# Optimization experiments

Hardware: AMD Instinct MI355X
Metric: run time of the kernel (lower is better)

The kernel has to match this reference:

```python
import jax, jax.numpy as jnp
import numpy as np

D_MODEL = 1024
N_HEADS = 16
D_FF = 4096
EPS = 1e-6


def _linear_params(key, d_in, d_out):
    kw, kb = jax.random.split(key)
    bound = 1.0 / np.sqrt(d_in)
    W = jax.random.uniform(kw, (d_out, d_in), minval=-bound, maxval=bound, dtype=jnp.float32)
    b = jax.random.uniform(kb, (d_out,), minval=-bound, maxval=bound, dtype=jnp.float32)
    return W, b


def setup_inputs() -> dict:
    key = jax.random.key(0)
    keys = jax.random.split(key, 8)
    x = jax.random.normal(keys[0], (4, 2048, D_MODEL), dtype=jnp.float32)
    mask = jnp.ones((4, 1, 1, 2048), dtype=jnp.bool_)
    Wq, bq = _linear_params(keys[1], D_MODEL, D_MODEL)
    Wk, bk = _linear_params(keys[2], D_MODEL, D_MODEL)
    Wv, bv = _linear_params(keys[3], D_MODEL, D_MODEL)
    Wo, bo = _linear_params(keys[4], D_MODEL, D_MODEL)
    W1, b1 = _linear_params(keys[5], D_MODEL, D_FF)
    W2, b2 = _linear_params(keys[6], D_FF, D_MODEL)
    ln1_g = jnp.ones((D_MODEL,), jnp.float32); ln1_b = jnp.zeros((D_MODEL,), jnp.float32)
    ln2_g = jnp.ones((D_MODEL,), jnp.float32); ln2_b = jnp.zeros((D_MODEL,), jnp.float32)
    return {"x": x, "mask": mask,
            "Wq": Wq, "bq": bq, "Wk": Wk, "bk": bk, "Wv": Wv, "bv": bv,
            "Wo": Wo, "bo": bo, "W1": W1, "b1": b1, "W2": W2, "b2": b2,
            "ln1_g": ln1_g, "ln1_b": ln1_b, "ln2_g": ln2_g, "ln2_b": ln2_b}


def _layernorm(x, g, b):
    # torch LayerNorm here uses unbiased std and divides by (std + eps)
    mean = jnp.mean(x, axis=-1, keepdims=True)
    std = jnp.std(x, axis=-1, keepdims=True, ddof=1)
    return g * (x - mean) / (std + EPS) + b


def _gelu_tanh(x):
    c = np.sqrt(2.0 / np.pi).astype(np.float32)
    return 0.5 * x * (1.0 + jnp.tanh(c * (x + 0.044715 * x * x * x)))


def _mha(xn, mask, Wq, bq, Wk, bk, Wv, bv, Wo, bo):
    B, S, D = xn.shape
    d_k = D // N_HEADS
    def proj(W, b):
        y = jnp.einsum('bsd,ed->bse', xn, W) + b
        return y.reshape(B, S, N_HEADS, d_k).transpose(0, 2, 1, 3)  # [B,h,S,d_k]
    q, k, v = proj(Wq, bq), proj(Wk, bk), proj(Wv, bv)
    scores = jnp.einsum('bhqd,bhkd->bhqk', q, k) / np.float32(np.sqrt(d_k))
    scores = jnp.where(mask, scores, jnp.float32(-1e9))
    p = jax.nn.softmax(scores, axis=-1)
    o = jnp.einsum('bhqk,bhkd->bhqd', p, v)
    o = o.transpose(0, 2, 1, 3).reshape(B, S, D)
    return jnp.einsum('bsd,ed->bse', o, Wo) + bo


def reference(x, mask, Wq, bq, Wk, bk, Wv, bv, Wo, bo, W1, b1, W2, b2,
              ln1_g, ln1_b, ln2_g, ln2_b):
    xn = _layernorm(x, ln1_g, ln1_b)
    y = x + _mha(xn, mask, Wq, bq, Wk, bk, Wv, bv, Wo, bo)
    yn = _layernorm(y, ln2_g, ln2_b)
    h = _gelu_tanh(jnp.einsum('bsd,fd->bsf', yn, W1) + b1)
    z = y + (jnp.einsum('bsf,df->bsd', h, W2) + b2)
    return z
```

## Files before the change

### kernel.cpp

```cpp
#include <hip/hip_runtime.h>

typedef __bf16 bf16;
typedef __bf16 bfx4 __attribute__((ext_vector_type(4)));
typedef __bf16 bfx8 __attribute__((ext_vector_type(8)));
typedef float  fx4  __attribute__((ext_vector_type(4)));

#define NTOK 8192
#define DM   1024
#define DFF  4096
#define SEQ  2048
#define NH   16
#define DK   64

#define OFF_WQKV 0ull
#define OFF_WO   (OFF_WQKV + 3072ull*1024*2)
#define OFF_W1   (OFF_WO   + 1024ull*1024*2)
#define OFF_W2   (OFF_W1   + 4096ull*1024*2)
#define OFF_BQKV (OFF_W2   + 4096ull*1024*2)
#define OFF_XN   (OFF_BQKV + 3072ull*4)
#define OFF_QKV  (OFF_XN   + 8192ull*1024*2)
#define OFF_ATTN (OFF_QKV  + 8192ull*3072*2)
#define OFF_Y    (OFF_ATTN + 8192ull*1024*2)
#define OFF_VT   OFF_Y
#define OFF_H    OFF_XN
#define OFF_YN   OFF_ATTN

#define BARRIER() do { asm volatile("" ::: "memory"); \
                       __builtin_amdgcn_s_barrier();  \
                       asm volatile("" ::: "memory"); } while (0)

__device__ __forceinline__ void gload16(const void* g, void* l) {
  __builtin_amdgcn_global_load_lds(
      (__attribute__((address_space(1))) void*)(g),
      (__attribute__((address_space(3))) void*)(l), 16, 0, 0);
}

__device__ __forceinline__ float gelu_tanh(float x) {
  float u = 0.7978845608028654f * (x + 0.044715f * x * x * x);
  float t = 1.f - 2.f / (__expf(2.f * u) + 1.f);
  return 0.5f * x * (1.f + t);
}

__global__ __launch_bounds__(256) void cast_all(const float* __restrict__ Wq,
                                                const float* __restrict__ Wk,
                                                const float* __restrict__ Wv,
                                                const float* __restrict__ Wo,
                                                const float* __restrict__ W1,
                                                const float* __restrict__ W2,
                                                bf16* __restrict__ dst) {
  const int bid = blockIdx.x;
  const int g = bid >> 9;
  const int j = ((bid & 511) << 11) + threadIdx.x * 8;
  const float* s;
  if (g == 0) s = Wq;
  else if (g == 1) s = Wk;
  else if (g == 2) s = Wv;
  else if (g == 3) s = Wo;
  else if (g < 8) s = W1 + (size_t)(g - 4) * 1048576;
  else s = W2 + (size_t)(g - 8) * 1048576;
  const float4 a = *(const float4*)(s + j);
  const float4 c = *(const float4*)(s + j + 4);
  bfx8 o;
  o[0] = (bf16)a.x; o[1] = (bf16)a.y; o[2] = (bf16)a.z; o[3] = (bf16)a.w;
  o[4] = (bf16)c.x; o[5] = (bf16)c.y; o[6] = (bf16)c.z; o[7] = (bf16)c.w;
  *(bfx8*)(dst + (size_t)g * 1048576 + j) = o;
}

__global__ void biask(const float* __restrict__ bq, const float* __restrict__ bk,
                      const float* __restrict__ bv, float* __restrict__ o) {
  const int i = blockIdx.x * 1024 + threadIdx.x;
  const float* s = blockIdx.x == 0 ? bq : (blockIdx.x == 1 ? bk : bv);
  o[i] = s[threadIdx.x];
}

__global__ __launch_bounds__(256) void ln_kernel(const float* __restrict__ x,
                                                 const float* __restrict__ g,
                                                 const float* __restrict__ b,
                                                 bf16* __restrict__ out) {
  const int row = blockIdx.x;
  const int c = threadIdx.x * 4;
  const float4 v = *(const float4*)&x[(size_t)row * DM + c];
  float s1 = v.x + v.y + v.z + v.w;
  float s2 = v.x * v.x + v.y * v.y + v.z * v.z + v.w * v.w;
  #pragma unroll
  for (int o = 32; o; o >>= 1) { s1 += __shfl_xor(s1, o); s2 += __shfl_xor(s2, o); }
  __shared__ float red[8];
  const int wid = threadIdx.x >> 6;
  if ((threadIdx.x & 63) == 0) { red[wid] = s1; red[4 + wid] = s2; }
  __syncthreads();
  s1 = red[0] + red[1] + red[2] + red[3];
  s2 = red[4] + red[5] + red[6] + red[7];
  const float mean = s1 * (1.f / (float)DM);
  const float var = (s2 - (float)DM * mean * mean) * (1.f / (float)(DM - 1));
  const float inv = 1.f / (sqrtf(fmaxf(var, 0.f)) + 1e-6f);
  bfx4 o;
  o[0] = (bf16)(g[c + 0] * (v.x - mean) * inv + b[c + 0]);
  o[1] = (bf16)(g[c + 1] * (v.y - mean) * inv + b[c + 1]);
  o[2] = (bf16)(g[c + 2] * (v.z - mean) * inv + b[c + 2]);
  o[3] = (bf16)(g[c + 3] * (v.w - mean) * inv + b[c + 3]);
  *(bfx4*)&out[(size_t)row * DM + c] = o;
}

template <int NREP, int EPI, int VSPLIT>
__global__ __launch_bounds__(512, 2) void gemm256(const bf16* __restrict__ A,
                                                  const bf16* __restrict__ B,
                                                  const float* __restrict__ bias,
                                                  const float* __restrict__ resid,
                                                  bf16* __restrict__ vt,
                                                  void* __restrict__ outp,
                                                  int M, int N, int K) {
  extern __shared__ char lds[];
  constexpr int BHALF = NREP * 4096;
  const int tid = threadIdx.x;
  const int lane = tid & 63, w = tid >> 6;
  const int l15 = lane & 15, lhi = lane >> 4;
  const int wm = w >> 2, wn = w & 3;

  const int nwg = gridDim.x * gridDim.y;
  int bid = blockIdx.y * gridDim.x + blockIdx.x;
  bid = (bid & 7) * (nwg >> 3) + (bid >> 3);
  const int m0 = (bid % gridDim.x) * 256;
  const int n0 = (bid / gridDim.x) * (NREP * 64);

  const char* Ab = (const char*)A;
  const char* Bb = (const char*)B;
  const size_t str = (size_t)K * 2;

  const int r_s = tid >> 3;
  const int c2  = (tid & 7) * 16;
  const int csw = c2 ^ ((r_s & 7) << 4);

  auto stA = [&](int buf, int half, int kt) {
    const size_t kb = (size_t)kt * 128;
    #pragma unroll
    for (int s = 0; s < 2; ++s)
      gload16(Ab + (size_t)(m0 + half * 128 + s * 64 + r_s) * str + kb + csw,
              lds + (buf * 2 + half) * 16384 + s * 8192 + tid * 16);
  };
  auto stB = [&](int buf, int half, int kt) {
    const size_t kb = (size_t)kt * 128;
    #pragma unroll
    for (int s = 0; s < NREP / 2; ++s)
      gload16(Bb + (size_t)(n0 + half * (NREP * 32) + s * 64 + r_s) * str + kb + csw,
              lds + 65536 + (buf * 2 + half) * BHALF + s * 8192 + tid * 16);
  };

  fx4 acc[8][NREP] = {};
  bfx8 af[4][2];
  bfx8 bfv[NREP][2];
  const int asw = (l15 & 7) << 4;

  auto ldA = [&](int buf, int i0) {
    const char* base = lds + (buf * 2 + wm) * 16384;
    #pragma unroll
    for (int ii = 0; ii < 4; ++ii) {
      const int r = (i0 + ii) * 16 + l15;
      #pragma unroll
      for (int kk = 0; kk < 2; ++kk)
        af[ii][kk] = *(const bfx8*)(base + r * 128 + ((kk * 64 + lhi * 16) ^ asw));
    }
  };
  auto ldB = [&](int buf, int j0) {
    const char* base = lds + 65536 + (buf * 2 + (wn >> 1)) * BHALF;
    #pragma unroll
    for (int jj = 0; jj < NREP / 2; ++jj) {
      const int r = (wn & 1) * (NREP * 16) + (j0 + jj) * 16 + l15;
      #pragma unroll
      for (int kk = 0; kk < 2; ++kk)
        bfv[j0 + jj][kk] = *(const bfx8*)(base + r * 128 + ((kk * 64 + lhi * 16) ^ asw));
    }
  };
  auto mm = [&](int qm, int qn) {
    __builtin_amdgcn_s_setprio(1);
    #pragma unroll
    for (int ii = 0; ii < 4; ++ii)
      #pragma unroll
      for (int jj = 0; jj < NREP / 2; ++jj)
        #pragma unroll
        for (int kk = 0; kk < 2; ++kk)
          acc[qm * 4 + ii][qn * (NREP / 2) + jj] =
              __builtin_amdgcn_mfma_f32_16x16x32_bf16(
                  af[ii][kk], bfv[qn * (NREP / 2) + jj][kk],
                  acc[qm * 4 + ii][qn * (NREP / 2) + jj], 0, 0, 0);
    __builtin_amdgcn_s_setprio(0);
  };

  const int nK = K >> 6, niters = nK >> 1;

  stA(0, 0, 0); stA(0, 1, 0); stB(0, 0, 0); stB(0, 1, 0);
  stB(1, 0, 1); stB(1, 1, 1);
  asm volatile("s_waitcnt vmcnt(%0)" :: "i"(NREP) : "memory");
  BARRIER();

  #pragma unroll 1
  for (int it = 0; it < niters; ++it) {
    const int t1 = 2 * it + 1, t2 = 2 * it + 2, t3 = 2 * it + 3;
    const bool more = (it < niters - 1);
    ldA(0, 0); ldB(0, 0);
    stA(1, 0, t1);
    BARRIER(); mm(0, 0); BARRIER();
    ldB(0, NREP / 2);
    stA(1, 1, t1);
    BARRIER(); mm(0, 1); BARRIER();
    ldA(0, 4);
    if (more) stB(0, 0, t2);
    BARRIER(); mm(1, 0); BARRIER();
    if (more) {
      stB(0, 1, t2);
      asm volatile("s_waitcnt vmcnt(%0)" :: "i"(NREP) : "memory");
    } else {
      asm volatile("s_waitcnt vmcnt(0)" ::: "memory");
    }
    BARRIER(); mm(1, 1); BARRIER();
    ldA(1, 0); ldB(1, 0);
    if (more) stA(0, 0, t2);
    BARRIER(); mm(0, 0); BARRIER();
    ldB(1, NREP / 2);
    if (more) stA(0, 1, t2);
    BARRIER(); mm(0, 1); BARRIER();
    ldA(1, 4);
    if (more) stB(1, 0, t3);
    BARRIER(); mm(1, 0); BARRIER();
    if (more) {
      stB(1, 1, t3);
      asm volatile("s_waitcnt vmcnt(%0)" :: "i"(NREP) : "memory");
    }
    BARRIER(); mm(1, 1); BARRIER();
  }

  const int rb = m0 + wm * 128 + lhi * 4;
  const int cb = n0 + wn * 16 * NREP + l15;
  #pragma unroll
  for (int j = 0; j < NREP; ++j) {
    const int c = cb + j * 16;
    const float bv = bias[c];
    if (VSPLIT && c >= 2048) {
      const int hd = c - 2048;
      #pragma unroll
      for (int i = 0; i < 8; ++i) {
        const int tok = rb + i * 16;
        const int bb = tok >> 11;
        bfx4 o4;
        #pragma unroll
        for (int e = 0; e < 4; ++e) o4[e] = (bf16)(acc[i][j][e] + bv);
        *(bfx4*)&vt[((size_t)(bb * 1024 + hd)) * SEQ + (tok & 2047)] = o4;
      }
    } else {
      #pragma unroll
      for (int i = 0; i < 8; ++i) {
        #pragma unroll
        for (int e = 0; e < 4; ++e) {
          const size_t idx = (size_t)(rb + i * 16 + e) * N + c;
          float v = acc[i][j][e] + bv;
          if constexpr (EPI == 1) v = gelu_tanh(v);
          if constexpr (EPI == 2) {
            ((float*)outp)[idx] = v + resid[idx];
          } else {
            ((bf16*)outp)[idx] = (bf16)v;
          }
        }
      }
    }
  }
}

__global__ __launch_bounds__(256, 4) void attn_kernel(const bf16* __restrict__ QKV,
                                                      const bf16* __restrict__ VT,
                                                      bf16* __restrict__ O) {
  __shared__ bf16 lds[2][2][4096];
  const int tid = threadIdx.x;
  const int lane = tid & 63, w = tid >> 6;
  const int l15 = lane & 15, lhi = lane >> 4;
  int id = blockIdx.x;
  id = (id & 7) * 128 + (id >> 3);
  const int q0 = (id & 15) * 128;
  const int h = (id >> 4) & 15;
  const int b = id >> 8;
  const size_t tokbase = (size_t)b * SEQ;

  const int lin0 = w * 1024 + lane * 16;
  const int lin1 = lin0 + 4096;
  const int row0 = lin0 >> 7, row1 = lin1 >> 7;
  const int cs0 = (lin0 & 127) ^ ((row0 & 7) << 4);
  const int cs1 = (lin1 & 127) ^ ((row1 & 7) << 4);
  const char* kp0 = (const char*)QKV + ((tokbase + row0) * 3072 + 1024 + h * 64) * 2 + cs0;
  const char* kp1 = (const char*)QKV + ((tokbase + row1) * 3072 + 1024 + h * 64) * 2 + cs1;
  const char* vbase = (const char*)(VT + (size_t)((b * NH + h) * 64) * SEQ);
  const char* vp0 = vbase + (size_t)row0 * (SEQ * 2) + cs0;
  const char* vp1 = vbase + (size_t)row1 * (SEQ * 2) + cs1;
  char* const ldsb = (char*)&lds[0][0][0];
  int dofs = 0;
  const long KADV = 64l * 3072 * 2;
  const long VADV = 64l * 2;

  auto stage = [&]() {
    gload16(kp0, ldsb + dofs + lin0);
    gload16(kp1, ldsb + dofs + lin1);
    gload16(vp0, ldsb + dofs + 8192 + lin0);
    gload16(vp1, ldsb + dofs + 8192 + lin1);
    kp0 += KADV; kp1 += KADV; vp0 += VADV; vp1 += VADV;
    dofs ^= 16384;
  };

  stage();

  bfx8 qf[2][2];
  #pragma unroll
  for (int m = 0; m < 2; ++m)
    #pragma unroll
    for (int kk = 0; kk < 2; ++kk) {
      bfx8 raw = *(const bfx8*)&QKV[(tokbase + q0 + w * 32 + m * 16 + l15) * 3072
                                    + h * DK + kk * 32 + lhi * 8];
      bfx8 sc;
      #pragma unroll
      for (int e = 0; e < 8; ++e) sc[e] = (bf16)((float)raw[e] * 0.18033688011112042f);
      qf[m][kk] = sc;
    }

  fx4 acc[2][4] = {};
  fx4 lsum[2] = {};
  bfx8 ones;
  #pragma unroll
  for (int e = 0; e < 8; ++e) ones[e] = (bf16)1.0f;

  const int NT = SEQ / 64;
  #pragma unroll 2
  for (int t = 0; t < NT; ++t) {
    if (t + 1 < NT) {
      stage();
      asm volatile("s_waitcnt vmcnt(4)" ::: "memory");
    } else {
      asm volatile("s_waitcnt vmcnt(0)" ::: "memory");
    }
    __builtin_amdgcn_s_barrier();

    const char* Kl = ldsb + ((t & 1) << 14);
    const char* Vl = Kl + 8192;

    fx4 s[2][4] = {};
    #pragma unroll
    for (int kk = 0; kk < 2; ++kk) {
      bfx8 kf[4];
      #pragma unroll
      for (int n = 0; n < 4; ++n) {
        const int row = n * 16 + l15;
        kf[n] = *(const bfx8*)(Kl + row * 128 + ((kk * 64 + lhi * 16) ^ ((row & 7) << 4)));
      }
      __builtin_amdgcn_s_setprio(1);
      #pragma unroll
      for (int m = 0; m < 2; ++m)
        #pragma unroll
        for (int n = 0; n < 4; ++n)
          s[m][n] = __builtin_amdgcn_mfma_f32_16x16x32_bf16(kf[n], qf[m][kk], s[m][n], 0, 0, 0);
      __builtin_amdgcn_s_setprio(0);
    }

    uint32_t pu[2][4][2];
    #pragma unroll
    for (int m = 0; m < 2; ++m)
      #pragma unroll
      for (int n = 0; n < 4; ++n) {
        const float p0 = exp2f(s[m][n][0]);
        const float p1 = exp2f(s[m][n][1]);
        const float p2 = exp2f(s[m][n][2]);
        const float p3 = exp2f(s[m][n][3]);
        union { bf16 h2[2]; uint32_t u; } c0, c1;
        c0.h2[0] = (bf16)p0; c0.h2[1] = (bf16)p1;
        c1.h2[0] = (bf16)p2; c1.h2[1] = (bf16)p3;
        pu[m][n][0] = c0.u; pu[m][n][1] = c1.u;
      }

    #pragma unroll
    for (int kk = 0; kk < 2; ++kk) {
      bfx8 pB[2];
      #pragma unroll
      for (int m = 0; m < 2; ++m) {
        union { uint32_t u[4]; bfx8 v; } cb2;
        cb2.u[0] = pu[m][2 * kk][0];
        cb2.u[1] = pu[m][2 * kk][1];
        cb2.u[2] = pu[m][2 * kk + 1][0];
        cb2.u[3] = pu[m][2 * kk + 1][1];
        pB[m] = cb2.v;
      }
      __builtin_amdgcn_s_setprio(1);
      #pragma unroll
      for (int m = 0; m < 2; ++m)
        lsum[m] = __builtin_amdgcn_mfma_f32_16x16x32_bf16(ones, pB[m], lsum[m], 0, 0, 0);
      __builtin_amdgcn_s_setprio(0);
      #pragma unroll
      for (int dn = 0; dn < 4; ++dn) {
        const int row = dn * 16 + l15;
        const int sw = (row & 7) << 4;
        union { bfx4 q2[2]; bfx8 v; } vv;
        vv.q2[0] = *(const bfx4*)(Vl + row * 128 + ((kk * 64 + lhi * 8) ^ sw));
        vv.q2[1] = *(const bfx4*)(Vl + row * 128 + ((kk * 64 + 32 + lhi * 8) ^ sw));
        __builtin_amdgcn_s_setprio(1);
        #pragma unroll
        for (int m = 0; m < 2; ++m)
          acc[m][dn] = __builtin_amdgcn_mfma_f32_16x16x32_bf16(vv.v, pB[m], acc[m][dn], 0, 0, 0);
        __builtin_amdgcn_s_setprio(0);
      }
    }

    asm volatile("s_waitcnt lgkmcnt(0)" ::: "memory");
    __builtin_amdgcn_s_barrier();
  }

  __syncthreads();
  bf16* Ep = &lds[0][0][0] + w * 2048;
  const float rinv0 = __builtin_amdgcn_rcpf(lsum[0][0]);
  const float rinv1 = __builtin_amdgcn_rcpf(lsum[1][0]);
  #pragma unroll
  for (int m = 0; m < 2; ++m) {
    const int qr = m * 16 + l15;
    const int sw = (qr & 7) << 4;
    const float ri = m ? rinv1 : rinv0;
    #pragma unroll
    for (int dn = 0; dn < 4; ++dn)
      #pragma unroll
      for (int e = 0; e < 4; ++e) {
        const int d = dn * 16 + lhi * 4 + e;
        *(bf16*)((char*)Ep + qr * 128 + ((2 * d) ^ sw)) = (bf16)(acc[m][dn][e] * ri);
      }
  }
  __syncthreads();
  #pragma unroll
  for (int j = 0; j < 4; ++j) {
    const int qr = lane >> 1;
    const int cbyte = (lane & 1) * 64 + j * 16;
    bfx8 v = *(const bfx8*)((char*)Ep + qr * 128 + (cbyte ^ ((qr & 7) << 4)));
    *(bfx8*)&O[(tokbase + q0 + w * 32 + qr) * (size_t)DM + h * DK + (lane & 1) * 32 + j * 8] = v;
  }
}

extern "C" void kernel_launch(void* const* d_in, const int* in_sizes, int n_in,
                              void* d_out, int out_size, void* d_ws, size_t ws_size,
                              hipStream_t stream) {
  const float* x  = (const float*)d_in[0];
  const float* Wq = (const float*)d_in[2];
  const float* bq = (const float*)d_in[3];
  const float* Wk = (const float*)d_in[4];
  const float* bk = (const float*)d_in[5];
  const float* Wv = (const float*)d_in[6];
  const float* bv = (const float*)d_in[7];
  const float* Wo = (const float*)d_in[8];
  const float* bo = (const float*)d_in[9];
  const float* W1 = (const float*)d_in[10];
  const float* b1 = (const float*)d_in[11];
  const float* W2 = (const float*)d_in[12];
  const float* b2 = (const float*)d_in[13];
  const float* g1 = (const float*)d_in[14];
  const float* be1 = (const float*)d_in[15];
  const float* g2 = (const float*)d_in[16];
  const float* be2 = (const float*)d_in[17];

  char* ws = (char*)d_ws;
  bf16* WQKVb = (bf16*)(ws + OFF_WQKV);
  bf16* WOb   = (bf16*)(ws + OFF_WO);
  bf16* W1b   = (bf16*)(ws + OFF_W1);
  bf16* W2b   = (bf16*)(ws + OFF_W2);
  float* BQKV = (float*)(ws + OFF_BQKV);
  bf16* XN    = (bf16*)(ws + OFF_XN);
  bf16* QKVb  = (bf16*)(ws + OFF_QKV);
  bf16* ATTNb = (bf16*)(ws + OFF_ATTN);
  float* Yb   = (float*)(ws + OFF_Y);
  bf16* VTb   = (bf16*)(ws + OFF_VT);
  bf16* Hb    = (bf16*)(ws + OFF_H);
  bf16* YNb   = (bf16*)(ws + OFF_YN);

  hipFuncSetAttribute((const void*)&gemm256<4, 0, 1>,
                      hipFuncAttributeMaxDynamicSharedMemorySize, 131072);
  hipFuncSetAttribute((const void*)&gemm256<4, 1, 0>,
                      hipFuncAttributeMaxDynamicSharedMemorySize, 131072);
  hipFuncSetAttribute((const void*)&gemm256<2, 2, 0>,
                      hipFuncAttributeMaxDynamicSharedMemorySize, 98304);

  cast_all<<<6144, 256, 0, stream>>>(Wq, Wk, Wv, Wo, W1, W2, WQKVb);
  biask<<<3, 1024, 0, stream>>>(bq, bk, bv, BQKV);

  ln_kernel<<<NTOK, 256, 0, stream>>>(x, g1, be1, XN);
  gemm256<4, 0, 1><<<dim3(32, 12), 512, 131072, stream>>>(XN, WQKVb, BQKV, nullptr,
                                                          VTb, QKVb, NTOK, 3072, 1024);
  attn_kernel<<<1024, 256, 0, stream>>>(QKVb, VTb, ATTNb);
  gemm256<2, 2, 0><<<dim3(32, 8), 512, 98304, stream>>>(ATTNb, WOb, bo, x, nullptr,
                                                        Yb, NTOK, 1024, 1024);
  ln_kernel<<<NTOK, 256, 0, stream>>>(Yb, g2, be2, YNb);
  gemm256<4, 1, 0><<<dim3(32, 16), 512, 131072, stream>>>(YNb, W1b, b1, nullptr,
                                                          nullptr, Hb, NTOK, 4096, 1024);
  gemm256<2, 2, 0><<<dim3(32, 8), 512, 98304, stream>>>(Hb, W2b, b2, Yb, nullptr,
                                                        (float*)d_out, NTOK, 1024, 4096);
}
```

Before: 426.3 us.

## Replace 256-row 8-wave GEMM with simple 128x128 double-buffered 4-wave GEMM

Swaps the hand-scheduled 256xN GEMM, which used 512 threads, 128KB of dynamic LDS and interleaved barriers, for a simpler 128x128 tile kernel. The new kernel uses 256 threads, 64KB of static LDS, a double buffer and one barrier per K-step, and all four GEMMs now run on the same tile shape. The aim is more workgroups per CU and less barrier overhead. In exchange, each tile reuses data less, so global and LDS traffic per FLOP rises, and the fine-grained overlap of loads with MFMA is lost.

```diff
diff --git a/kernel.cpp b/kernel.cpp
--- a/kernel.cpp
+++ b/kernel.cpp
@@ -24,10 +24,6 @@
 #define OFF_VT   OFF_Y
 #define OFF_H    OFF_XN
 #define OFF_YN   OFF_ATTN
-
-#define BARRIER() do { asm volatile("" ::: "memory"); \
-                       __builtin_amdgcn_s_barrier();  \
-                       asm volatile("" ::: "memory"); } while (0)
 
 __device__ __forceinline__ void gload16(const void* g, void* l) {
   __builtin_amdgcn_global_load_lds(
@@ -101,143 +97,90 @@
   *(bfx4*)&out[(size_t)row * DM + c] = o;
 }
 
-template <int NREP, int EPI, int VSPLIT>
-__global__ __launch_bounds__(512, 2) void gemm256(const bf16* __restrict__ A,
-                                                  const bf16* __restrict__ B,
-                                                  const float* __restrict__ bias,
-                                                  const float* __restrict__ resid,
-                                                  bf16* __restrict__ vt,
-                                                  void* __restrict__ outp,
-                                                  int M, int N, int K) {
-  extern __shared__ char lds[];
-  constexpr int BHALF = NREP * 4096;
+template <int EPI, int VSPLIT>
+__global__ __launch_bounds__(256) void gemmdp(const bf16* __restrict__ A,
+                                              const bf16* __restrict__ B,
+                                              const float* __restrict__ bias,
+                                              const float* __restrict__ resid,
+                                              bf16* __restrict__ vt,
+                                              void* __restrict__ outp,
+                                              int M, int N, int K) {
+  __shared__ char lds[65536];
   const int tid = threadIdx.x;
   const int lane = tid & 63, w = tid >> 6;
   const int l15 = lane & 15, lhi = lane >> 4;
-  const int wm = w >> 2, wn = w & 3;
+  const int wm = w >> 1, wn = w & 1;
 
   const int nwg = gridDim.x * gridDim.y;
   int bid = blockIdx.y * gridDim.x + blockIdx.x;
   bid = (bid & 7) * (nwg >> 3) + (bid >> 3);
-  const int m0 = (bid % gridDim.x) * 256;
-  const int n0 = (bid / gridDim.x) * (NREP * 64);
-
-  const char* Ab = (const char*)A;
-  const char* Bb = (const char*)B;
+  const int m0 = (bid % gridDim.x) * 128;
+  const int n0 = (bid / gridDim.x) * 128;
   const size_t str = (size_t)K * 2;
 
   const int r_s = tid >> 3;
   const int c2  = (tid & 7) * 16;
   const int csw = c2 ^ ((r_s & 7) << 4);
-
-  auto stA = [&](int buf, int half, int kt) {
-    const size_t kb = (size_t)kt * 128;
-    #pragma unroll
-    for (int s = 0; s < 2; ++s)
-      gload16(Ab + (size_t)(m0 + half * 128 + s * 64 + r_s) * str + kb + csw,
-              lds + (buf * 2 + half) * 16384 + s * 8192 + tid * 16);
+  const char* ap = (const char*)A + (size_t)(m0 + r_s) * str + csw;
+  const char* bp = (const char*)B + (size_t)(n0 + r_s) * str + csw;
+
+  auto stage = [&](int buf) {
+    char* dst = lds + buf * 32768 + tid * 16;
+    #pragma unroll
+    for (int s = 0; s < 4; ++s)
+      gload16(ap + (size_t)(s * 32) * str, dst + s * 4096);
+    #pragma unroll
+    for (int s = 0; s < 4; ++s)
+      gload16(bp + (size_t)(s * 32) * str, dst + 16384 + s * 4096);
+    ap += 128; bp += 128;
   };
-  auto stB = [&](int buf, int half, int kt) {
-    const size_t kb = (size_t)kt * 128;
-    #pragma unroll
-    for (int s = 0; s < NREP / 2; ++s)
-      gload16(Bb + (size_t)(n0 + half * (NREP * 32) + s * 64 + r_s) * str + kb + csw,
-              lds + 65536 + (buf * 2 + half) * BHALF + s * 8192 + tid * 16);
-  };
-
-  fx4 acc[8][NREP] = {};
-  bfx8 af[4][2];
-  bfx8 bfv[NREP][2];
+
+  fx4 acc[4][4] = {};
   const int asw = (l15 & 7) << 4;
-
-  auto ldA = [&](int buf, int i0) {
-    const char* base = lds + (buf * 2 + wm) * 16384;
-    #pragma unroll
-    for (int ii = 0; ii < 4; ++ii) {
-      const int r = (i0 + ii) * 16 + l15;
-      #pragma unroll
-      for (int kk = 0; kk < 2; ++kk)
-        af[ii][kk] = *(const bfx8*)(base + r * 128 + ((kk * 64 + lhi * 16) ^ asw));
-    }
-  };
-  auto ldB = [&](int buf, int j0) {
-    const char* base = lds + 65536 + (buf * 2 + (wn >> 1)) * BHALF;
-    #pragma unroll
-    for (int jj = 0; jj < NREP / 2; ++jj) {
-      const int r = (wn & 1) * (NREP * 16) + (j0 + jj) * 16 + l15;
-      #pragma unroll
-      for (int kk = 0; kk < 2; ++kk)
-        bfv[j0 + jj][kk] = *(const bfx8*)(base + r * 128 + ((kk * 64 + lhi * 16) ^ asw));
-    }
-  };
-  auto mm = [&](int qm, int qn) {
-    __builtin_amdgcn_s_setprio(1);
-    #pragma unroll
-    for (int ii = 0; ii < 4; ++ii)
-      #pragma unroll
-      for (int jj = 0; jj < NREP / 2; ++jj)
+  const int nK = K >> 6;
+
+  stage(0);
+
+  #pragma unroll 1
+  for (int t = 0; t < nK; ++t) {
+    asm volatile("s_waitcnt vmcnt(0)" ::: "memory");
+    __builtin_amdgcn_s_barrier();
+    asm volatile("" ::: "memory");
+    if (t + 1 < nK) stage((t + 1) & 1);
+
+    const char* Ab = lds + (t & 1) * 32768;
+    const char* Bb = Ab + 16384;
+    #pragma unroll
+    for (int kk = 0; kk < 2; ++kk) {
+      bfx8 af[4], bv[4];
+      #pragma unroll
+      for (int i = 0; i < 4; ++i)
+        af[i] = *(const bfx8*)(Ab + (wm * 64 + i * 16 + l15) * 128 +
+                               ((kk * 64 + lhi * 16) ^ asw));
+      #pragma unroll
+      for (int j = 0; j < 4; ++j)
+        bv[j] = *(const bfx8*)(Bb + (wn * 64 + j * 16 + l15) * 128 +
+                               ((kk * 64 + lhi * 16) ^ asw));
+      __builtin_amdgcn_s_setprio(1);
+      #pragma unroll
+      for (int i = 0; i < 4; ++i)
         #pragma unroll
-        for (int kk = 0; kk < 2; ++kk)
-          acc[qm * 4 + ii][qn * (NREP / 2) + jj] =
-              __builtin_amdgcn_mfma_f32_16x16x32_bf16(
-                  af[ii][kk], bfv[qn * (NREP / 2) + jj][kk],
-                  acc[qm * 4 + ii][qn * (NREP / 2) + jj], 0, 0, 0);
-    __builtin_amdgcn_s_setprio(0);
-  };
-
-  const int nK = K >> 6, niters = nK >> 1;
-
-  stA(0, 0, 0); stA(0, 1, 0); stB(0, 0, 0); stB(0, 1, 0);
-  stB(1, 0, 1); stB(1, 1, 1);
-  asm volatile("s_waitcnt vmcnt(%0)" :: "i"(NREP) : "memory");
-  BARRIER();
-
-  #pragma unroll 1
-  for (int it = 0; it < niters; ++it) {
-    const int t1 = 2 * it + 1, t2 = 2 * it + 2, t3 = 2 * it + 3;
-    const bool more = (it < niters - 1);
-    ldA(0, 0); ldB(0, 0);
-    stA(1, 0, t1);
-    BARRIER(); mm(0, 0); BARRIER();
-    ldB(0, NREP / 2);
-    stA(1, 1, t1);
-    BARRIER(); mm(0, 1); BARRIER();
-    ldA(0, 4);
-    if (more) stB(0, 0, t2);
-    BARRIER(); mm(1, 0); BARRIER();
-    if (more) {
-      stB(0, 1, t2);
-      asm volatile("s_waitcnt vmcnt(%0)" :: "i"(NREP) : "memory");
-    } else {
-      asm volatile("s_waitcnt vmcnt(0)" ::: "memory");
-    }
-    BARRIER(); mm(1, 1); BARRIER();
-    ldA(1, 0); ldB(1, 0);
-    if (more) stA(0, 0, t2);
-    BARRIER(); mm(0, 0); BARRIER();
-    ldB(1, NREP / 2);
-    if (more) stA(0, 1, t2);
-    BARRIER(); mm(0, 1); BARRIER();
-    ldA(1, 4);
-    if (more) stB(1, 0, t3);
-    BARRIER(); mm(1, 0); BARRIER();
-    if (more) {
-      stB(1, 1, t3);
-      asm volatile("s_waitcnt vmcnt(%0)" :: "i"(NREP) : "memory");
-    }
-    BARRIER(); mm(1, 1); BARRIER();
+        for (int j = 0; j < 4; ++j)
+          acc[i][j] = __builtin_amdgcn_mfma_f32_16x16x32_bf16(af[i], bv[j], acc[i][j], 0, 0, 0);
+      __builtin_amdgcn_s_setprio(0);
+    }
   }
 
-  const int rb = m0 + wm * 128 + lhi * 4;
-  const int cb = n0 + wn * 16 * NREP + l15;
-  #pragma unroll
-  for (int j = 0; j < NREP; ++j) {
+  const int rb = m0 + wm * 64 + lhi * 4;
+  const int cb = n0 + wn * 64 + l15;
+  #pragma unroll
+  for (int j = 0; j < 4; ++j) {
     const int c = cb + j * 16;
     const float bv = bias[c];
     if (VSPLIT && c >= 2048) {
       const int hd = c - 2048;
       #pragma unroll
-      for (int i = 0; i < 8; ++i) {
+      for (int i = 0; i < 4; ++i) {
         const int tok = rb + i * 16;
         const int bb = tok >> 11;
         bfx4 o4;
@@ -247,7 +190,7 @@
       }
     } else {
       #pragma unroll
-      for (int i = 0; i < 8; ++i) {
+      for (int i = 0; i < 4; ++i) {
         #pragma unroll
         for (int e = 0; e < 4; ++e) {
           const size_t idx = (size_t)(rb + i * 16 + e) * N + c;
@@ -468,25 +411,18 @@
   bf16* Hb    = (bf16*)(ws + OFF_H);
   bf16* YNb   = (bf16*)(ws + OFF_YN);
 
-  hipFuncSetAttribute((const void*)&gemm256<4, 0, 1>,
-                      hipFuncAttributeMaxDynamicSharedMemorySize, 131072);
-  hipFuncSetAttribute((const void*)&gemm256<4, 1, 0>,
-                      hipFuncAttributeMaxDynamicSharedMemorySize, 131072);
-  hipFuncSetAttribute((const void*)&gemm256<2, 2, 0>,
-                      hipFuncAttributeMaxDynamicSharedMemorySize, 98304);
-
   cast_all<<<6144, 256, 0, stream>>>(Wq, Wk, Wv, Wo, W1, W2, WQKVb);
   biask<<<3, 1024, 0, stream>>>(bq, bk, bv, BQKV);
 
   ln_kernel<<<NTOK, 256, 0, stream>>>(x, g1, be1, XN);
-  gemm256<4, 0, 1><<<dim3(32, 12), 512, 131072, stream>>>(XN, WQKVb, BQKV, nullptr,
-                                                          VTb, QKVb, NTOK, 3072, 1024);
+  gemmdp<0, 1><<<dim3(64, 24), 256, 0, stream>>>(XN, WQKVb, BQKV, nullptr,
+                                                 VTb, QKVb, NTOK, 3072, 1024);
   attn_kernel<<<1024, 256, 0, stream>>>(QKVb, VTb, ATTNb);
-  gemm256<2, 2, 0><<<dim3(32, 8), 512, 98304, stream>>>(ATTNb, WOb, bo, x, nullptr,
-                                                        Yb, NTOK, 1024, 1024);
+  gemmdp<2, 0><<<dim3(64, 8), 256, 0, stream>>>(ATTNb, WOb, bo, x, nullptr,
+                                                Yb, NTOK, 1024, 1024);
   ln_kernel<<<NTOK, 256, 0, stream>>>(Yb, g2, be2, YNb);
-  gemm256<4, 1, 0><<<dim3(32, 16), 512, 131072, stream>>>(YNb, W1b, b1, nullptr,
-                                                          nullptr, Hb, NTOK, 4096, 1024);
-  gemm256<2, 2, 0><<<dim3(32, 8), 512, 98304, stream>>>(Hb, W2b, b2, Yb, nullptr,
-                                                        (float*)d_out, NTOK, 1024, 4096);
-}
+  gemmdp<1, 0><<<dim3(64, 32), 256, 0, stream>>>(YNb, W1b, b1, nullptr,
+                                                 nullptr, Hb, NTOK, 4096, 1024);
+  gemmdp<2, 0><<<dim3(64, 8), 256, 0, stream>>>(Hb, W2b, b2, Yb, nullptr,
+                                                (float*)d_out, NTOK, 1024, 4096);
+}
```

Result: slower. 442.2 us (+3.7%).
